# Optimization experiments

Measured on AMD Instinct MI355X. Metric: run time of the kernel, lower is better.

## Reference

```python
import jax, jax.numpy as jnp
import numpy as np

B, N, D, H, DK, DV = 2, 2048, 1024, 16, 64, 64


def setup_inputs() -> dict:
    key = jax.random.key(0)
    k1, k2, k3, k4, k5 = jax.random.split(key, 5)
    X = jax.random.normal(k1, (B, N, D), dtype=jnp.float32)
    W_Q = jax.random.normal(k2, (H, D, DK), dtype=jnp.float32) * 0.02
    W_K = jax.random.normal(k3, (H, D, DK), dtype=jnp.float32) * 0.02
    W_V = jax.random.normal(k4, (H, D, DV), dtype=jnp.float32) * 0.02
    W_O = jax.random.normal(k5, (H * DV, D), dtype=jnp.float32) * 0.02
    return {"X": X, "W_Q": W_Q, "W_K": W_K, "W_V": W_V, "W_O": W_O}


def reference(X, W_Q, W_K, W_V, W_O):
    # Per-head projections: X [b,n,d] x W [h,d,k] -> [b,h,n,k]
    Q = jnp.einsum('bik,hkj->bhij', X, W_Q)
    K = jnp.einsum('bik,hkj->bhij', X, W_K)
    V = jnp.einsum('bik,hkj->bhij', X, W_V)
    # Scores [b,h,n,n] -- NOTE: original applies no 1/sqrt(d_k) scale and no causal mask
    QKT = jnp.einsum('bhik,bhjk->bhij', Q, K)
    # Original softmaxes over dim=2 (the QUERY axis), reproduced literally
    A = jax.nn.softmax(QKT, axis=2)
    AV = jnp.einsum('bhik,bhkj->bhij', A, V)  # [b,h,n,dv]
    # Literal reshape (b,h,n,dv)->(b,n,h*dv) without transpose, as in torch.reshape
    AV_concat = jnp.reshape(AV, (B, N, H * DV))
    SA_out = jnp.einsum('bni,id->bnd', AV_concat, W_O)
    return SA_out
```

## Files before the change

kernel.cpp:

```cpp
#include <hip/hip_runtime.h>
#include <math.h>

namespace {

typedef unsigned short u16;
typedef unsigned int   u32;
typedef __bf16 bf16x8 __attribute__((ext_vector_type(8)));
typedef float  f32x4  __attribute__((ext_vector_type(4)));
typedef float  f32x16 __attribute__((ext_vector_type(16)));
typedef u32    u32x4  __attribute__((ext_vector_type(4)));

constexpr size_t OFF_XH  = 0;
constexpr size_t OFF_WH  = 4194304;
constexpr size_t OFF_WL  = 7340032;
constexpr size_t OFF_QH  = 10485760;
constexpr size_t OFF_QL  = 14680064;
constexpr size_t OFF_KH  = 18874368;
constexpr size_t OFF_VT  = 23068672;
constexpr size_t OFF_WOT = 27262976;
constexpr size_t OFF_L   = 28311552;
constexpr size_t OFF_AVH = 0;

constexpr size_t VT_ELEMS = (size_t)32 * 64 * 2048;

__device__ __forceinline__ u16 f2bf(float x) {
  union { float f; unsigned u; } v; v.f = x;
  unsigned r = v.u + 0x7FFFu + ((v.u >> 16) & 1u);
  return (u16)(r >> 16);
}
__device__ __forceinline__ float bf2f(u16 b) {
  union { unsigned u; float f; } v; v.u = (unsigned)b << 16; return v.f;
}
__device__ __forceinline__ bf16x8 frag(const u16* p) {
  return *reinterpret_cast<const bf16x8*>(p);
}
__device__ __forceinline__ f32x4 mfma16(bf16x8 a, bf16x8 b, f32x4 c) {
  return __builtin_amdgcn_mfma_f32_16x16x32_bf16(a, b, c, 0, 0, 0);
}
__device__ __forceinline__ f32x16 mfma32(bf16x8 a, bf16x8 b, f32x16 c) {
  return __builtin_amdgcn_mfma_f32_32x32x16_bf16(a, b, c, 0, 0, 0);
}
__device__ __forceinline__ void gload16(const void* g, void* l) {
  __builtin_amdgcn_global_load_lds(
      (const __attribute__((address_space(1))) u32*)g,
      (__attribute__((address_space(3))) u32*)l, 16, 0, 0);
}
__device__ __forceinline__ u32 cvtpk(float lo, float hi) {
  u32 r;
  asm("v_cvt_pk_bf16_f32 %0, %1, %2" : "=v"(r) : "v"(lo), "v"(hi));
  return r;
}
__device__ __forceinline__ void pswap(u32& a, u32& b) {
  asm("v_permlane32_swap_b32 %0, %1" : "+v"(a), "+v"(b));
}

__global__ __launch_bounds__(256) void k_prep_x(
    const float* __restrict__ X, u16* __restrict__ wsu)
{
  u16* Xh = wsu + OFF_XH;
  const size_t i = ((size_t)blockIdx.x * 256 + threadIdx.x) * 4;
  const float4 v = *(const float4*)&X[i];
  ushort4 hh;
  hh.x = f2bf(v.x); hh.y = f2bf(v.y); hh.z = f2bf(v.z); hh.w = f2bf(v.w);
  *(ushort4*)&Xh[i] = hh;
  if (blockIdx.x < 64) {
    float* L = (float*)(wsu + OFF_L);
    const size_t li = ((size_t)blockIdx.x * 256 + threadIdx.x) * 4;
    *(float4*)&L[li] = make_float4(0.f, 0.f, 0.f, 0.f);
  }
}

__global__ __launch_bounds__(256) void k_prep_w(
    const float* __restrict__ Wq, const float* __restrict__ Wk,
    const float* __restrict__ Wv, const float* __restrict__ Wo,
    u16* __restrict__ wsu)
{
  const int bx = blockIdx.x;
  const int tid = threadIdx.x;
  __shared__ float T[64][65];
  if (bx < 768) {
    const int qkv = bx >> 8, h = (bx >> 4) & 15, dc = bx & 15;
    const float* W = qkv == 0 ? Wq : qkv == 1 ? Wk : Wv;
    const int d0 = dc * 64;
    for (int l = 0; l < 16; ++l) {
      int idx = tid + l * 256; int r = idx >> 6, c = idx & 63;
      T[r][c] = W[((size_t)h * 1024 + d0 + r) * 64 + c];
    }
    __syncthreads();
    u16* Wh = wsu + OFF_WH;
    u16* Wl = wsu + OFF_WL;
    for (int l = 0; l < 16; ++l) {
      int idx = tid + l * 256; int r = idx >> 6, c = idx & 63;
      float v = T[c][r];
      u16 hi = f2bf(v);
      size_t o = (size_t)((qkv * 16 + h) * 64 + r) * 1024 + d0 + c;
      Wh[o] = hi;
      Wl[o] = f2bf(v - bf2f(hi));
    }
  } else {
    const int b2 = bx - 768;
    const int c0 = (b2 >> 4) * 64, dd0 = (b2 & 15) * 64;
    for (int l = 0; l < 16; ++l) {
      int idx = tid + l * 256; int r = idx >> 6, c = idx & 63;
      T[r][c] = Wo[(size_t)(c0 + r) * 1024 + dd0 + c];
    }
    __syncthreads();
    u16* WOT = wsu + OFF_WOT;
    for (int l = 0; l < 16; ++l) {
      int idx = tid + l * 256; int r = idx >> 6, c = idx & 63;
      WOT[(size_t)(dd0 + r) * 1024 + c0 + c] = f2bf(T[c][r]);
    }
  }
}

__global__ __launch_bounds__(256, 2) void k_projg(u16* __restrict__ wsu)
{
  const int bid = blockIdx.x;
  const int xcd = bid & 7, local = bid >> 3;
  const int ct = xcd * 6 + (local % 6);
  const int mt = local / 6;
  const int gm0 = mt * 128;
  const int j0 = ct * 64;
  const int qkv = ct >> 4, h = ct & 15;

  const u16* XH = wsu + OFF_XH;
  const u16* WH = wsu + OFF_WH;
  const u16* WL = wsu + OFF_WL;

  __shared__ __align__(16) u16 lds[16384];
  u16* Ah = lds;
  u16* Bh = lds + 8192;
  u16* Bl = lds + 12288;

  const int tid = threadIdx.x;
  const int w = tid >> 6, l = tid & 63, lr = l & 15, lg = l >> 4;
  const int wm = w >> 1, wn = w & 1;

  const f32x4 fz = {0.f, 0.f, 0.f, 0.f};
  f32x4 acc[4][2];
  for (int i = 0; i < 4; ++i) for (int j = 0; j < 2; ++j) acc[i][j] = fz;

  for (int kt = 0; kt < 16; ++kt) {
    const int d0 = kt * 64;
    __syncthreads();
    #pragma unroll
    for (int it = 0; it < 8; ++it) {
      const int c = tid + it * 256;
      const u16* src;
      if (c < 1024) {
        const int r = c >> 3, col8 = (c & 7) * 8;
        src = XH + (size_t)(gm0 + r) * 1024 + d0 + col8;
      } else {
        const int cc = c - 1024;
        const int plane = cc >> 9, c2 = cc & 511;
        const int r = c2 >> 3, col8 = (c2 & 7) * 8;
        src = (plane ? WL : WH) + (size_t)(j0 + r) * 1024 + d0 + col8;
      }
      gload16(src, lds + (size_t)c * 8);
    }
    __syncthreads();

    #pragma unroll
    for (int ks = 0; ks < 2; ++ks) {
      bf16x8 a_h[4], b_h[2], b_l[2];
      #pragma unroll
      for (int mf = 0; mf < 4; ++mf) {
        const int row = wm * 64 + mf * 16 + lr;
        a_h[mf] = frag(Ah + row * 64 + ks * 32 + lg * 8);
      }
      #pragma unroll
      for (int nf = 0; nf < 2; ++nf) {
        const int row = wn * 32 + nf * 16 + lr;
        b_h[nf] = frag(Bh + row * 64 + ks * 32 + lg * 8);
        b_l[nf] = frag(Bl + row * 64 + ks * 32 + lg * 8);
      }
      #pragma unroll
      for (int nf = 0; nf < 2; ++nf)
        #pragma unroll
        for (int mf = 0; mf < 4; ++mf) {
          acc[mf][nf] = mfma16(a_h[mf], b_h[nf], acc[mf][nf]);
          acc[mf][nf] = mfma16(a_h[mf], b_l[nf], acc[mf][nf]);
        }
    }
  }

  if (qkv == 0) {
    u16* Ph = wsu + OFF_QH;
    u16* Pl = wsu + OFF_QL;
    #pragma unroll
    for (int mf = 0; mf < 4; ++mf)
      #pragma unroll
      for (int nf = 0; nf < 2; ++nf)
        #pragma unroll
        for (int r = 0; r < 4; ++r) {
          const float v = acc[mf][nf][r];
          const int gn = gm0 + wm * 64 + mf * 16 + lg * 4 + r;
          const int b = gn >> 11, n = gn & 2047;
          const int kp = wn * 32 + nf * 16 + lr;
          const size_t o = ((size_t)(b * 16 + h) * 2048 + n) * 64 + kp;
          const u16 hi = f2bf(v);
          Ph[o] = hi;
          Pl[o] = f2bf(v - bf2f(hi));
        }
  } else if (qkv == 1) {
    u16* Ph = wsu + OFF_KH;
    #pragma unroll
    for (int mf = 0; mf < 4; ++mf)
      #pragma unroll
      for (int nf = 0; nf < 2; ++nf)
        #pragma unroll
        for (int r = 0; r < 4; ++r) {
          const int gn = gm0 + wm * 64 + mf * 16 + lg * 4 + r;
          const int b = gn >> 11, n = gn & 2047;
          const int kp = wn * 32 + nf * 16 + lr;
          Ph[((size_t)(b * 16 + h) * 2048 + n) * 64 + kp] = f2bf(acc[mf][nf][r]);
        }
  } else {
    u16* VT = wsu + OFF_VT;
    #pragma unroll
    for (int mf = 0; mf < 4; ++mf)
      #pragma unroll
      for (int nf = 0; nf < 2; ++nf) {
        const int gn = gm0 + wm * 64 + mf * 16 + lg * 4;
        const int b = gn >> 11, n = gn & 2047;
        const int kp = wn * 32 + nf * 16 + lr;
        ushort4 p;
        p.x = f2bf(acc[mf][nf][0]); p.y = f2bf(acc[mf][nf][1]);
        p.z = f2bf(acc[mf][nf][2]); p.w = f2bf(acc[mf][nf][3]);
        *(ushort4*)&VT[((size_t)(b * 16 + h) * 64 + kp) * 2048 + n] = p;
      }
  }
}

__global__ __launch_bounds__(256, 2) void k_pass1(
    u16* __restrict__ wsu, float* __restrict__ L)
{
  const int bid = blockIdx.x;
  const int swz = (bid & 7) * 256 + (bid >> 3);
  const int bh = swz >> 6;
  const int jtile = (swz >> 2) & 15;
  const int isl = swz & 3;
  const int j0 = jtile * 128;
  const u16* Qh = wsu + OFF_QH + (size_t)bh * 131072;
  const u16* Ql = wsu + OFF_QL + (size_t)bh * 131072;
  const u16* Kh = wsu + OFF_KH + (size_t)bh * 131072;

  __shared__ __align__(16) u16 lds[2][2][4096];

  const int tid = threadIdx.x;
  const int w = tid >> 6, l = tid & 63;
  const int il = l & 31, hi = l >> 5;

  bf16x8 kah[4];
  {
    const int jrow = j0 + w * 32 + il;
    #pragma unroll
    for (int ks = 0; ks < 4; ++ks)
      kah[ks] = frag(&Kh[(size_t)jrow * 64 + ks * 16 + hi * 8]);
  }

  auto stage = [&](int buf, int ic) {
    const int i0 = ic * 64;
    #pragma unroll
    for (int it = 0; it < 4; ++it) {
      const int c = tid + it * 256;
      const int plane = c >> 9, cc = c & 511;
      const int r = cc >> 3, cl = cc & 7;
      const int sw8 = (cl ^ (r & 7)) * 8;
      const u16* src = (plane ? Ql : Qh) + (size_t)(i0 + r) * 64 + sw8;
      gload16(src, &lds[buf][0][0] + (size_t)c * 8);
    }
  };

  const f32x16 fz16 = {0,0,0,0,0,0,0,0,0,0,0,0,0,0,0,0};
  float lsum[16] = {};
  const int icbase = isl * 8;

  stage(0, icbase);
  __syncthreads();
  int cur = 0;
  for (int ii = 0; ii < 8; ++ii) {
    if (ii < 7) stage(cur ^ 1, icbase + ii + 1);
    const u16* Qsh = &lds[cur][0][0];
    const u16* Qsl = &lds[cur][1][0];
    #pragma unroll
    for (int it2 = 0; it2 < 2; ++it2) {
      f32x16 s = fz16;
      const int qrow = it2 * 32 + il;
      #pragma unroll
      for (int ks = 0; ks < 4; ++ks) {
        const int ch = ((ks * 2 + hi) ^ (qrow & 7)) * 8;
        s = mfma32(kah[ks], frag(&Qsh[qrow * 64 + ch]), s);
        s = mfma32(kah[ks], frag(&Qsl[qrow * 64 + ch]), s);
      }
      #pragma unroll
      for (int r = 0; r < 16; ++r) lsum[r] += __expf(s[r]);
    }
    __syncthreads();
    cur ^= 1;
  }

  #pragma unroll
  for (int r = 0; r < 16; ++r) {
    float v = lsum[r];
    v += __shfl_xor(v, 1);  v += __shfl_xor(v, 2);
    v += __shfl_xor(v, 4);  v += __shfl_xor(v, 8);
    v += __shfl_xor(v, 16);
    if (il == 0) {
      const int j = j0 + w * 32 + (r & 3) + 8 * (r >> 2) + 4 * hi;
      atomicAdd(&L[(size_t)bh * 2048 + j], v);
    }
  }
}

__global__ __launch_bounds__(256) void k_scale_v(
    u16* __restrict__ wsu, const float* __restrict__ L)
{
  u16* VT = wsu + OFF_VT;
  const size_t vid = (size_t)blockIdx.x * 256 + threadIdx.x;
  if (vid * 8 >= VT_ELEMS) return;
  const size_t base = vid * 8;
  const int n8 = (int)(vid & 255);
  const int bh = (int)(vid >> 14);
  ushort4 a = *(ushort4*)&VT[base];
  ushort4 b = *(ushort4*)&VT[base + 4];
  const float* Lp = L + (size_t)bh * 2048 + n8 * 8;
  a.x = f2bf(bf2f(a.x) * __builtin_amdgcn_rcpf(Lp[0]));
  a.y = f2bf(bf2f(a.y) * __builtin_amdgcn_rcpf(Lp[1]));
  a.z = f2bf(bf2f(a.z) * __builtin_amdgcn_rcpf(Lp[2]));
  a.w = f2bf(bf2f(a.w) * __builtin_amdgcn_rcpf(Lp[3]));
  b.x = f2bf(bf2f(b.x) * __builtin_amdgcn_rcpf(Lp[4]));
  b.y = f2bf(bf2f(b.y) * __builtin_amdgcn_rcpf(Lp[5]));
  b.z = f2bf(bf2f(b.z) * __builtin_amdgcn_rcpf(Lp[6]));
  b.w = f2bf(bf2f(b.w) * __builtin_amdgcn_rcpf(Lp[7]));
  *(ushort4*)&VT[base] = a;
  *(ushort4*)&VT[base + 4] = b;
}

__global__ __launch_bounds__(256, 2) void k_pass2(u16* __restrict__ wsu)
{
  const int bid = blockIdx.x;
  const int swz = (bid & 7) * 64 + (bid >> 3);
  const int itile = swz & 15, bh = swz >> 4;
  const int i0 = itile * 128;
  const u16* Qh = wsu + OFF_QH + (size_t)bh * 131072;
  const u16* Ql = wsu + OFF_QL + (size_t)bh * 131072;
  const u16* Kh = wsu + OFF_KH + (size_t)bh * 131072;
  const u16* VT = wsu + OFF_VT + (size_t)bh * 131072;

  __shared__ __align__(16) u16 lds[2][2][4096];

  const int tid = threadIdx.x;
  const int w = tid >> 6, l = tid & 63;
  const int il = l & 31, hi = l >> 5;

  bf16x8 qbh[4], qbl[4];
  {
    const int irow = i0 + w * 32 + il;
    #pragma unroll
    for (int ks = 0; ks < 4; ++ks) {
      const size_t o = (size_t)irow * 64 + ks * 16 + hi * 8;
      qbh[ks] = frag(&Qh[o]);
      qbl[ks] = frag(&Ql[o]);
    }
  }

  auto stage = [&](int buf, int jc) {
    const int j0 = jc * 64;
    #pragma unroll
    for (int it = 0; it < 4; ++it) {
      const int c = tid + it * 256;
      const int plane = c >> 9, cc = c & 511;
      const int r = cc >> 3, cl = cc & 7;
      const int sw8 = (cl ^ (r & 7)) * 8;
      const u16* src = plane == 0 ? Kh + (size_t)(j0 + r) * 64 + sw8
                                  : VT + (size_t)r * 2048 + j0 + sw8;
      gload16(src, &lds[buf][0][0] + (size_t)c * 8);
    }
  };

  const f32x16 fz16 = {0,0,0,0,0,0,0,0,0,0,0,0,0,0,0,0};
  f32x16 acc[2]; acc[0] = fz16; acc[1] = fz16;

  stage(0, 0);
  __syncthreads();
  int cur = 0;
  for (int jc = 0; jc < 32; ++jc) {
    if (jc < 31) stage(cur ^ 1, jc + 1);
    const u16* Ksh = &lds[cur][0][0];
    const u16* Vs  = &lds[cur][1][0];
    #pragma unroll
    for (int jt = 0; jt < 2; ++jt) {
      f32x16 s = fz16;
      const int jrow = jt * 32 + il;
      #pragma unroll
      for (int ks = 0; ks < 4; ++ks) {
        const int ch = ((ks * 2 + hi) ^ (jrow & 7)) * 8;
        bf16x8 ka = frag(&Ksh[jrow * 64 + ch]);
        s = mfma32(ka, qbh[ks], s);
        s = mfma32(ka, qbl[ks], s);
      }
      float p[16];
      #pragma unroll
      for (int r = 0; r < 16; ++r) p[r] = __expf(s[r]);
      u32 a0 = cvtpk(p[0],  p[1]),  b0 = cvtpk(p[4],  p[5]);
      u32 a1 = cvtpk(p[2],  p[3]),  b1 = cvtpk(p[6],  p[7]);
      u32 a2 = cvtpk(p[8],  p[9]),  b2 = cvtpk(p[12], p[13]);
      u32 a3 = cvtpk(p[10], p[11]), b3 = cvtpk(p[14], p[15]);
      pswap(a0, b0); pswap(a1, b1); pswap(a2, b2); pswap(a3, b3);
      u32x4 pw0 = {a0, a1, b0, b1};
      u32x4 pw1 = {a2, a3, b2, b3};
      bf16x8 pa0 = __builtin_bit_cast(bf16x8, pw0);
      bf16x8 pa1 = __builtin_bit_cast(bf16x8, pw1);
      #pragma unroll
      for (int cb = 0; cb < 2; ++cb) {
        const int crow = cb * 32 + il;
        const int c0 = ((jt * 4 + 0 + hi) ^ (crow & 7)) * 8;
        const int c1 = ((jt * 4 + 2 + hi) ^ (crow & 7)) * 8;
        bf16x8 vb0 = frag(&Vs[crow * 64 + c0]);
        bf16x8 vb1 = frag(&Vs[crow * 64 + c1]);
        acc[cb] = mfma32(pa0, vb0, acc[cb]);
        acc[cb] = mfma32(pa1, vb1, acc[cb]);
      }
    }
    __syncthreads();
    cur ^= 1;
  }

  u16* AVh = wsu + OFF_AVH;
  #pragma unroll
  for (int cb = 0; cb < 2; ++cb)
    #pragma unroll
    for (int r = 0; r < 16; ++r) {
      const int iloc = (r & 3) + 8 * (r >> 2) + 4 * hi;
      const int g = i0 + w * 32 + iloc;
      const int c = cb * 32 + il;
      AVh[((size_t)bh * 2048 + g) * 64 + c] = f2bf(acc[cb][r]);
    }
}

__global__ __launch_bounds__(256, 2) void k_outproj(
    const u16* __restrict__ wsu, float* __restrict__ Out)
{
  const int bx = blockIdx.x;
  const int gm = bx >> 3, dn = bx & 7;
  const int g0 = gm * 128, d0 = dn * 128;
  const u16* AVh = wsu + OFF_AVH;
  const u16* WOT = wsu + OFF_WOT;

  __shared__ __align__(16) u16 lds[16384];
  u16* As = lds;
  u16* Bs = lds + 8192;

  const int tid = threadIdx.x;
  const int w = tid >> 6, l = tid & 63, lr = l & 15, lg = l >> 4;
  const int wm = w >> 1, wn = w & 1;

  const f32x4 fz = {0.f, 0.f, 0.f, 0.f};
  f32x4 acc[4][4];
  for (int i = 0; i < 4; ++i) for (int j = 0; j < 4; ++j) acc[i][j] = fz;

  for (int kt = 0; kt < 16; ++kt) {
    const int c0 = kt * 64;
    __syncthreads();
    #pragma unroll
    for (int it = 0; it < 8; ++it) {
      const int c = tid + it * 256;
      const u16* src;
      if (c < 1024) {
        const int r = c >> 3, col8 = (c & 7) * 8;
        src = AVh + (size_t)(g0 + r) * 1024 + c0 + col8;
      } else {
        const int cc = c - 1024;
        const int r = cc >> 3, col8 = (cc & 7) * 8;
        src = WOT + (size_t)(d0 + r) * 1024 + c0 + col8;
      }
      gload16(src, lds + (size_t)c * 8);
    }
    __syncthreads();
    #pragma unroll
    for (int ks = 0; ks < 2; ++ks) {
      bf16x8 ah[4];
      #pragma unroll
      for (int mf = 0; mf < 4; ++mf)
        ah[mf] = frag(As + (wm * 64 + mf * 16 + lr) * 64 + ks * 32 + lg * 8);
      #pragma unroll
      for (int nf = 0; nf < 4; ++nf) {
        bf16x8 bfv = frag(Bs + (wn * 64 + nf * 16 + lr) * 64 + ks * 32 + lg * 8);
        #pragma unroll
        for (int mf = 0; mf < 4; ++mf)
          acc[mf][nf] = mfma16(ah[mf], bfv, acc[mf][nf]);
      }
    }
  }
  #pragma unroll
  for (int mf = 0; mf < 4; ++mf)
    #pragma unroll
    for (int nf = 0; nf < 4; ++nf)
      #pragma unroll
      for (int r = 0; r < 4; ++r) {
        const int g = g0 + wm * 64 + mf * 16 + lg * 4 + r;
        const int d = d0 + wn * 64 + nf * 16 + lr;
        Out[(size_t)g * 1024 + d] = acc[mf][nf][r];
      }
}

}

extern "C" void kernel_launch(void* const* d_in, const int* in_sizes, int n_in,
                              void* d_out, int out_size, void* d_ws, size_t ws_size,
                              hipStream_t stream) {
  const float* X  = (const float*)d_in[0];
  const float* Wq = (const float*)d_in[1];
  const float* Wk = (const float*)d_in[2];
  const float* Wv = (const float*)d_in[3];
  const float* Wo = (const float*)d_in[4];
  float* out = (float*)d_out;
  u16* wsu = (u16*)d_ws;
  float* L = (float*)(wsu + OFF_L);

  k_prep_x  <<<4096, 256, 0, stream>>>(X, wsu);
  k_prep_w  <<<1024, 256, 0, stream>>>(Wq, Wk, Wv, Wo, wsu);
  k_projg   <<<1536, 256, 0, stream>>>(wsu);
  k_pass1   <<<2048, 256, 0, stream>>>(wsu, L);
  k_scale_v <<<2048, 256, 0, stream>>>(wsu, L);
  k_pass2   <<<512,  256, 0, stream>>>(wsu);
  k_outproj <<<256,  256, 0, stream>>>(wsu, out);
}
```

Baseline: 210.7 us.

## Double-buffer and swizzle LDS in projection and out-projection GEMMs, widen proj tile

Both the QKV projection and output projection GEMMs now use two LDS buffers, so the next k-tile's global loads are issued before computing the current tile, with one barrier per step. LDS tiles use an XOR swizzle on 16-byte chunks to reduce bank conflicts on fragment reads. The projection tile is widened from 64 to 128 columns and the hi/lo weight planes become separate k-steps, so the launch uses 768 blocks instead of 1536. The cost is double the LDS per block, which may lower occupancy, and more accumulator registers.

Result: faster. 201.5 us (-4.3%).

```diff
diff --git a/kernel.cpp b/kernel.cpp
--- a/kernel.cpp
+++ b/kernel.cpp
@@ -117,86 +117,90 @@
 {
   const int bid = blockIdx.x;
   const int xcd = bid & 7, local = bid >> 3;
-  const int ct = xcd * 6 + (local % 6);
-  const int mt = local / 6;
+  const int ct = xcd * 3 + local % 3;
+  const int mt = local / 3;
   const int gm0 = mt * 128;
-  const int j0 = ct * 64;
-  const int qkv = ct >> 4, h = ct & 15;
+  const int j0 = ct * 128;
+  const int qkv = ct >> 3;
 
   const u16* XH = wsu + OFF_XH;
   const u16* WH = wsu + OFF_WH;
   const u16* WL = wsu + OFF_WL;
 
-  __shared__ __align__(16) u16 lds[16384];
-  u16* Ah = lds;
-  u16* Bh = lds + 8192;
-  u16* Bl = lds + 12288;
+  __shared__ __align__(16) u16 lds[2][16384];
 
   const int tid = threadIdx.x;
   const int w = tid >> 6, l = tid & 63, lr = l & 15, lg = l >> 4;
   const int wm = w >> 1, wn = w & 1;
 
-  const f32x4 fz = {0.f, 0.f, 0.f, 0.f};
-  f32x4 acc[4][2];
-  for (int i = 0; i < 4; ++i) for (int j = 0; j < 2; ++j) acc[i][j] = fz;
-
-  for (int kt = 0; kt < 16; ++kt) {
-    const int d0 = kt * 64;
-    __syncthreads();
+  auto stage = [&](int buf, int t) {
+    const int d0 = (t >> 1) * 64;
+    const u16* Wp = (t & 1) ? WL : WH;
     #pragma unroll
     for (int it = 0; it < 8; ++it) {
       const int c = tid + it * 256;
       const u16* src;
       if (c < 1024) {
-        const int r = c >> 3, col8 = (c & 7) * 8;
-        src = XH + (size_t)(gm0 + r) * 1024 + d0 + col8;
+        const int r = c >> 3, cl = c & 7;
+        src = XH + (size_t)(gm0 + r) * 1024 + d0 + (cl ^ (r & 7)) * 8;
       } else {
         const int cc = c - 1024;
-        const int plane = cc >> 9, c2 = cc & 511;
-        const int r = c2 >> 3, col8 = (c2 & 7) * 8;
-        src = (plane ? WL : WH) + (size_t)(j0 + r) * 1024 + d0 + col8;
-      }
-      gload16(src, lds + (size_t)c * 8);
-    }
-    __syncthreads();
-
+        const int r = cc >> 3, cl = cc & 7;
+        src = Wp + (size_t)(j0 + r) * 1024 + d0 + (cl ^ (r & 7)) * 8;
+      }
+      gload16(src, &lds[buf][0] + (size_t)c * 8);
+    }
+  };
+
+  const f32x4 fz = {0.f, 0.f, 0.f, 0.f};
+  f32x4 acc[4][4];
+  for (int i = 0; i < 4; ++i) for (int j = 0; j < 4; ++j) acc[i][j] = fz;
+
+  stage(0, 0);
+  __syncthreads();
+  int cur = 0;
+  for (int t = 0; t < 32; ++t) {
+    if (t < 31) stage(cur ^ 1, t + 1);
+    const u16* As = &lds[cur][0];
+    const u16* Bs = &lds[cur][8192];
     #pragma unroll
     for (int ks = 0; ks < 2; ++ks) {
-      bf16x8 a_h[4], b_h[2], b_l[2];
+      bf16x8 a[4], b[4];
       #pragma unroll
       for (int mf = 0; mf < 4; ++mf) {
         const int row = wm * 64 + mf * 16 + lr;
-        a_h[mf] = frag(Ah + row * 64 + ks * 32 + lg * 8);
-      }
-      #pragma unroll
-      for (int nf = 0; nf < 2; ++nf) {
-        const int row = wn * 32 + nf * 16 + lr;
-        b_h[nf] = frag(Bh + row * 64 + ks * 32 + lg * 8);
-        b_l[nf] = frag(Bl + row * 64 + ks * 32 + lg * 8);
-      }
-      #pragma unroll
-      for (int nf = 0; nf < 2; ++nf)
+        a[mf] = frag(As + row * 64 + ((ks * 4 + lg) ^ (row & 7)) * 8);
+      }
+      #pragma unroll
+      for (int nf = 0; nf < 4; ++nf) {
+        const int row = wn * 64 + nf * 16 + lr;
+        b[nf] = frag(Bs + row * 64 + ((ks * 4 + lg) ^ (row & 7)) * 8);
+      }
+      #pragma unroll
+      for (int nf = 0; nf < 4; ++nf)
         #pragma unroll
-        for (int mf = 0; mf < 4; ++mf) {
-          acc[mf][nf] = mfma16(a_h[mf], b_h[nf], acc[mf][nf]);
-          acc[mf][nf] = mfma16(a_h[mf], b_l[nf], acc[mf][nf]);
-        }
-    }
-  }
-
+        for (int mf = 0; mf < 4; ++mf)
+          acc[mf][nf] = mfma16(a[mf], b[nf], acc[mf][nf]);
+    }
+    __syncthreads();
+    cur ^= 1;
+  }
+
+  const int colbase = j0 + wn * 64;
+  const int h = (colbase >> 6) & 15;
   if (qkv == 0) {
     u16* Ph = wsu + OFF_QH;
     u16* Pl = wsu + OFF_QL;
     #pragma unroll
     for (int mf = 0; mf < 4; ++mf)
       #pragma unroll
-      for (int nf = 0; nf < 2; ++nf)
+      for (int nf = 0; nf < 4; ++nf)
         #pragma unroll
         for (int r = 0; r < 4; ++r) {
           const float v = acc[mf][nf][r];
           const int gn = gm0 + wm * 64 + mf * 16 + lg * 4 + r;
           const int b = gn >> 11, n = gn & 2047;
-          const int kp = wn * 32 + nf * 16 + lr;
+          const int kp = nf * 16 + lr;
           const size_t o = ((size_t)(b * 16 + h) * 2048 + n) * 64 + kp;
           const u16 hi = f2bf(v);
           Ph[o] = hi;
@@ -207,12 +211,12 @@
     #pragma unroll
     for (int mf = 0; mf < 4; ++mf)
       #pragma unroll
-      for (int nf = 0; nf < 2; ++nf)
+      for (int nf = 0; nf < 4; ++nf)
         #pragma unroll
         for (int r = 0; r < 4; ++r) {
           const int gn = gm0 + wm * 64 + mf * 16 + lg * 4 + r;
           const int b = gn >> 11, n = gn & 2047;
-          const int kp = wn * 32 + nf * 16 + lr;
+          const int kp = nf * 16 + lr;
           Ph[((size_t)(b * 16 + h) * 2048 + n) * 64 + kp] = f2bf(acc[mf][nf][r]);
         }
   } else {
@@ -220,10 +224,10 @@
     #pragma unroll
     for (int mf = 0; mf < 4; ++mf)
       #pragma unroll
-      for (int nf = 0; nf < 2; ++nf) {
+      for (int nf = 0; nf < 4; ++nf) {
         const int gn = gm0 + wm * 64 + mf * 16 + lg * 4;
         const int b = gn >> 11, n = gn & 2047;
-        const int kp = wn * 32 + nf * 16 + lr;
+        const int kp = nf * 16 + lr;
         ushort4 p;
         p.x = f2bf(acc[mf][nf][0]); p.y = f2bf(acc[mf][nf][1]);
         p.z = f2bf(acc[mf][nf][2]); p.w = f2bf(acc[mf][nf][3]);
@@ -448,50 +452,62 @@
   const u16* AVh = wsu + OFF_AVH;
   const u16* WOT = wsu + OFF_WOT;
 
-  __shared__ __align__(16) u16 lds[16384];
-  u16* As = lds;
-  u16* Bs = lds + 8192;
+  __shared__ __align__(16) u16 lds[2][16384];
 
   const int tid = threadIdx.x;
   const int w = tid >> 6, l = tid & 63, lr = l & 15, lg = l >> 4;
   const int wm = w >> 1, wn = w & 1;
 
-  const f32x4 fz = {0.f, 0.f, 0.f, 0.f};
-  f32x4 acc[4][4];
-  for (int i = 0; i < 4; ++i) for (int j = 0; j < 4; ++j) acc[i][j] = fz;
-
-  for (int kt = 0; kt < 16; ++kt) {
-    const int c0 = kt * 64;
-    __syncthreads();
+  auto stage = [&](int buf, int t) {
+    const int c0 = t * 64;
     #pragma unroll
     for (int it = 0; it < 8; ++it) {
       const int c = tid + it * 256;
       const u16* src;
       if (c < 1024) {
-        const int r = c >> 3, col8 = (c & 7) * 8;
-        src = AVh + (size_t)(g0 + r) * 1024 + c0 + col8;
+        const int r = c >> 3, cl = c & 7;
+        src = AVh + (size_t)(g0 + r) * 1024 + c0 + (cl ^ (r & 7)) * 8;
       } else {
         const int cc = c - 1024;
-        const int r = cc >> 3, col8 = (cc & 7) * 8;
-        src = WOT + (size_t)(d0 + r) * 1024 + c0 + col8;
-      }
-      gload16(src, lds + (size_t)c * 8);
-    }
-    __syncthreads();
+        const int r = cc >> 3, cl = cc & 7;
+        src = WOT + (size_t)(d0 + r) * 1024 + c0 + (cl ^ (r & 7)) * 8;
+      }
+      gload16(src, &lds[buf][0] + (size_t)c * 8);
+    }
+  };
+
+  const f32x4 fz = {0.f, 0.f, 0.f, 0.f};
+  f32x4 acc[4][4];
+  for (int i = 0; i < 4; ++i) for (int j = 0; j < 4; ++j) acc[i][j] = fz;
+
+  stage(0, 0);
+  __syncthreads();
+  int cur = 0;
+  for (int t = 0; t < 16; ++t) {
+    if (t < 15) stage(cur ^ 1, t + 1);
+    const u16* As = &lds[cur][0];
+    const u16* Bs = &lds[cur][8192];
     #pragma unroll
     for (int ks = 0; ks < 2; ++ks) {
-      bf16x8 ah[4];
-      #pragma unroll
-      for (int mf = 0; mf < 4; ++mf)
-        ah[mf] = frag(As + (wm * 64 + mf * 16 + lr) * 64 + ks * 32 + lg * 8);
+      bf16x8 a[4], b[4];
+      #pragma unroll
+      for (int mf = 0; mf < 4; ++mf) {
+        const int row = wm * 64 + mf * 16 + lr;
+        a[mf] = frag(As + row * 64 + ((ks * 4 + lg) ^ (row & 7)) * 8);
+      }
       #pragma unroll
       for (int nf = 0; nf < 4; ++nf) {
-        bf16x8 bfv = frag(Bs + (wn * 64 + nf * 16 + lr) * 64 + ks * 32 + lg * 8);
+        const int row = wn * 64 + nf * 16 + lr;
+        b[nf] = frag(Bs + row * 64 + ((ks * 4 + lg) ^ (row & 7)) * 8);
+      }
+      #pragma unroll
+      for (int nf = 0; nf < 4; ++nf)
         #pragma unroll
         for (int mf = 0; mf < 4; ++mf)
-          acc[mf][nf] = mfma16(ah[mf], bfv, acc[mf][nf]);
-      }
-    }
+          acc[mf][nf] = mfma16(a[mf], b[nf], acc[mf][nf]);
+    }
+    __syncthreads();
+    cur ^= 1;
   }
   #pragma unroll
   for (int mf = 0; mf < 4; ++mf)
@@ -521,7 +537,7 @@
 
   k_prep_x  <<<4096, 256, 0, stream>>>(X, wsu);
   k_prep_w  <<<1024, 256, 0, stream>>>(Wq, Wk, Wv, Wo, wsu);
-  k_projg   <<<1536, 256, 0, stream>>>(wsu);
+  k_projg   <<<768,  256, 0, stream>>>(wsu);
   k_pass1   <<<2048, 256, 0, stream>>>(wsu, L);
   k_scale_v <<<2048, 256, 0, stream>>>(wsu, L);
   k_pass2   <<<512,  256, 0, stream>>>(wsu);
```
